# Kernel tuning notes

Measured on AMD Instinct MI355X. Metric: run time of the kernel, lower is better.

Reference implementation:

```python
import jax, jax.numpy as jnp
import numpy as np

D_MODEL = 768
N_HEADS = 12
D_HEAD = D_MODEL // N_HEADS
D_FF = 3072
EPS = 1e-5


def setup_inputs() -> dict:
    key = jax.random.key(0)
    ks = jax.random.split(key, 12)
    s = 0.02
    return {
        "x": jax.random.normal(ks[0], (2, 2048, D_MODEL), dtype=jnp.float32),
        "ln1_g": jnp.ones((D_MODEL,), jnp.float32),
        "ln1_b": jnp.zeros((D_MODEL,), jnp.float32),
        "ln2_g": jnp.ones((D_MODEL,), jnp.float32),
        "ln2_b": jnp.zeros((D_MODEL,), jnp.float32),
        "w_qkv": jax.random.normal(ks[1], (D_MODEL, 3 * D_MODEL), jnp.float32) * s,
        "b_qkv": jnp.zeros((3 * D_MODEL,), jnp.float32),
        "w_out": jax.random.normal(ks[2], (D_MODEL, D_MODEL), jnp.float32) * s,
        "b_out": jnp.zeros((D_MODEL,), jnp.float32),
        "w_fc1": jax.random.normal(ks[3], (D_MODEL, D_FF), jnp.float32) * s,
        "b_fc1": jnp.zeros((D_FF,), jnp.float32),
        "w_fc2": jax.random.normal(ks[4], (D_FF, D_MODEL), jnp.float32) * s,
        "b_fc2": jnp.zeros((D_MODEL,), jnp.float32),
    }


def _layernorm(x, g, b):
    mu = jnp.mean(x, axis=-1, keepdims=True)
    var = jnp.var(x, axis=-1, keepdims=True)
    return (x - mu) * jax.lax.rsqrt(var + EPS) * g + b


def _attention(h, w_qkv, b_qkv, w_out, b_out):
    B, S, _ = h.shape
    qkv = h @ w_qkv + b_qkv  # [B,S,3D]
    qkv = qkv.reshape(B, S, 3, N_HEADS, D_HEAD)
    q, k, v = qkv[:, :, 0], qkv[:, :, 1], qkv[:, :, 2]  # [B,S,H,Dh]
    scale = 1.0 / np.sqrt(D_HEAD).astype(np.float32)
    scores = jnp.einsum("bqhd,bkhd->bhqk", q, k) * scale
    causal = jnp.tril(jnp.ones((S, S), bool))
    scores = jnp.where(causal[None, None], scores, -jnp.inf)
    attn = jax.nn.softmax(scores, axis=-1)
    out = jnp.einsum("bhqk,bkhd->bqhd", attn, v).reshape(B, S, D_MODEL)
    return out @ w_out + b_out


def reference(x, ln1_g, ln1_b, ln2_g, ln2_b, w_qkv, b_qkv, w_out, b_out,
              w_fc1, b_fc1, w_fc2, b_fc2):
    # x = x + Attention(LN1(x))
    x = x + _attention(_layernorm(x, ln1_g, ln1_b), w_qkv, b_qkv, w_out, b_out)
    # x = x + FFN(LN2(x)); GELU is exact (erf) to match torch nn.GELU default
    h = _layernorm(x, ln2_g, ln2_b)
    h = jax.nn.gelu(h @ w_fc1 + b_fc1, approximate=False) @ w_fc2 + b_fc2
    return x + h
```

## Files before the change

### kernel.cpp

```cpp
#include <hip/hip_runtime.h>
#include <hip/hip_bf16.h>

typedef unsigned short u16;
typedef unsigned int u32;
typedef unsigned char u8;
using short8 = __attribute__((ext_vector_type(8))) short;
using f32x4  = __attribute__((ext_vector_type(4))) float;
using float4v = __attribute__((ext_vector_type(4))) float;

__device__ __forceinline__ u16 f2bf(float f) {
    __hip_bfloat16 h = __float2bfloat16(f);
    union { __hip_bfloat16 h; u16 u; } cv; cv.h = h; return cv.u;
}
__device__ __forceinline__ float bf2f(u16 u) {
    union { u32 u; float f; } cv; cv.u = ((u32)u) << 16; return cv.f;
}
__device__ __forceinline__ u16 f2bf_trunc(float f) {
    union { float f; u32 u; } cv; cv.f = f; return (u16)(cv.u >> 16);
}

__device__ __forceinline__ void gload_lds16(const void* g, void* l) {
    __builtin_amdgcn_global_load_lds(
        (const __attribute__((address_space(1))) u32*)g,
        (__attribute__((address_space(3))) u32*)l, 16, 0, 0);
}

__device__ __forceinline__ int xcd_remap(int flat, int nwg) {
    int q = nwg >> 3, r = nwg & 7;
    int xcd = flat & 7, pos = flat >> 3;
    int start = xcd < r ? xcd * (q + 1) : r * (q + 1) + (xcd - r) * q;
    return start + pos;
}

__global__ __launch_bounds__(256) void transpose_w(const float* __restrict__ W,
                                                   u16* __restrict__ Wt, int K, int N) {
    __shared__ float tile[32][33];
    int n0 = blockIdx.x * 32, k0 = blockIdx.y * 32;
    int tx = threadIdx.x & 31, ty = threadIdx.x >> 5;
    for (int i = 0; i < 4; i++) {
        int k = ty + i * 8;
        tile[k][tx] = W[(long)(k0 + k) * N + n0 + tx];
    }
    __syncthreads();
    for (int i = 0; i < 4; i++) {
        int n = ty + i * 8;
        Wt[(long)(n0 + n) * K + k0 + tx] = f2bf(tile[tx][n]);
    }
}

__global__ __launch_bounds__(256) void transpose_v(const u16* __restrict__ qkv,
                                                   u16* __restrict__ Vt) {
    __shared__ u16 tile[64][72];
    int s0 = blockIdx.x * 64;
    int bh = blockIdx.y;
    int b = bh / 12, h = bh % 12;
    int tid = threadIdx.x;
    const u16* src = qkv + (long)b * 2048 * 2304 + 1536 + h * 64;
    #pragma unroll
    for (int j = 0; j < 2; ++j) {
        int c = tid + j * 256;
        int srow = c >> 3, ch = c & 7;
        *(short8*)&tile[srow][ch * 8] = *(const short8*)(src + (long)(s0 + srow) * 2304 + ch * 8);
    }
    __syncthreads();
    u16* dst = Vt + (long)bh * 64 * 2048 + s0;
    #pragma unroll
    for (int j = 0; j < 2; ++j) {
        int c = tid + j * 256;
        int d = c >> 3, ch = c & 7;
        short8 v;
        #pragma unroll
        for (int e = 0; e < 8; ++e) v[e] = (short)tile[ch * 8 + e][d];
        *(short8*)(dst + (long)d * 2048 + ch * 8) = v;
    }
}

__global__ __launch_bounds__(256) void ln_kernel(const float* __restrict__ x,
                                                 const float* __restrict__ gain,
                                                 const float* __restrict__ beta,
                                                 u16* __restrict__ out) {
    int row = blockIdx.x;
    const float* xr = x + (long)row * 768;
    int tid = threadIdx.x;
    float v[3];
    float s = 0.f, s2 = 0.f;
    for (int j = 0; j < 3; j++) {
        v[j] = xr[tid + 256 * j];
        s += v[j]; s2 += v[j] * v[j];
    }
    for (int off = 32; off; off >>= 1) {
        s  += __shfl_down(s, off);
        s2 += __shfl_down(s2, off);
    }
    __shared__ float ws[8];
    int lane = tid & 63, w = tid >> 6;
    if (lane == 0) { ws[w] = s; ws[4 + w] = s2; }
    __syncthreads();
    s  = ws[0] + ws[1] + ws[2] + ws[3];
    s2 = ws[4] + ws[5] + ws[6] + ws[7];
    float mu  = s * (1.f / 768.f);
    float var = s2 * (1.f / 768.f) - mu * mu;
    float rs  = rsqrtf(var + 1e-5f);
    for (int j = 0; j < 3; j++) {
        int c = tid + 256 * j;
        out[(long)row * 768 + c] = f2bf((v[j] - mu) * rs * gain[c] + beta[c]);
    }
}

template <int EPI>
__global__ __launch_bounds__(256) void gemm_bf16(const u16* __restrict__ A, int lda,
                                                 const u16* __restrict__ Bt, int ldb,
                                                 const float* __restrict__ bias,
                                                 const float* __restrict__ res,
                                                 void* __restrict__ Cout0,
                                                 void* __restrict__ Cout1,
                                                 int M, int N, int K, int nN) {
    __shared__ alignas(16) u16 As[2][128 * 32];
    __shared__ alignas(16) u16 Bs[2][128 * 32];
    int nwg = gridDim.x;
    int wgid = xcd_remap(blockIdx.x, nwg);
    int tN = (wgid % nN) * 128, tM = (wgid / nN) * 128;
    int z = blockIdx.z;
    const u16* Ab = A + (long)z * K;
    const u16* Bb = Bt + (long)z * K;
    void* Cw = z ? Cout1 : Cout0;
    int tid = threadIdx.x;
    int wid = tid >> 6, lane = tid & 63;
    int wm = wid >> 1, wn = wid & 1;
    int g = lane >> 4, r = lane & 15;
    int srow = tid >> 2;
    int scol = tid & 3;

    f32x4 acc[4][4] = {};
    int KT = K >> 5;

    auto stage = [&](int kt) {
        int k0 = kt << 5;
        u16* ab = As[kt & 1];
        u16* bb = Bs[kt & 1];
        #pragma unroll
        for (int j = 0; j < 2; ++j) {
            int row = j * 64 + srow;
            int slot = scol ^ (row & 3);
            gload_lds16(Ab + (long)(tM + row) * lda + k0 + slot * 8, ab + (j * 64 + wid * 16) * 32);
            gload_lds16(Bb + (long)(tN + row) * ldb + k0 + slot * 8, bb + (j * 64 + wid * 16) * 32);
        }
    };

    stage(0);
    for (int kt = 0; kt < KT; ++kt) {
        if (kt + 1 < KT) {
            stage(kt + 1);
            asm volatile("s_waitcnt vmcnt(4)" ::: "memory");
        } else {
            asm volatile("s_waitcnt vmcnt(0)" ::: "memory");
        }
        __builtin_amdgcn_sched_barrier(0);
        __builtin_amdgcn_s_barrier();
        const u16* ab = As[kt & 1];
        const u16* bb = Bs[kt & 1];

        short8 af[4], bf[4];
        #pragma unroll
        for (int mi = 0; mi < 4; ++mi) {
            int row = wm * 64 + mi * 16 + r;
            af[mi] = *(const short8*)(ab + row * 32 + ((g ^ (row & 3)) * 8));
        }
        #pragma unroll
        for (int ni = 0; ni < 4; ++ni) {
            int row = wn * 64 + ni * 16 + r;
            bf[ni] = *(const short8*)(bb + row * 32 + ((g ^ (row & 3)) * 8));
        }
        #pragma unroll
        for (int mi = 0; mi < 4; ++mi)
            #pragma unroll
            for (int ni = 0; ni < 4; ++ni)
                acc[mi][ni] = __builtin_amdgcn_mfma_f32_16x16x32_bf16(af[mi], bf[ni], acc[mi][ni], 0, 0, 0);
        __builtin_amdgcn_s_barrier();
    }

    #pragma unroll
    for (int mi = 0; mi < 4; mi++) {
        #pragma unroll
        for (int ni = 0; ni < 4; ni++) {
            int col = tN + wn * 64 + ni * 16 + r;
            float bv = (EPI == 3) ? 0.f : bias[col];
            #pragma unroll
            for (int reg = 0; reg < 4; reg++) {
                int row = tM + wm * 64 + mi * 16 + g * 4 + reg;
                float v = acc[mi][ni][reg] + bv;
                if (EPI == 1) {
                    v += res[(long)row * N + col];
                    ((float*)Cw)[(long)row * N + col] = v;
                } else if (EPI == 2) {
                    v = 0.5f * v * (1.f + erff(v * 0.70710678118f));
                    ((u16*)Cw)[(long)row * N + col] = f2bf(v);
                } else if (EPI == 3) {
                    ((float*)Cw)[(long)row * N + col] = v;
                } else {
                    ((u16*)Cw)[(long)row * N + col] = f2bf(v);
                }
            }
        }
    }
}

__global__ __launch_bounds__(192) void fc2_combine(const float* __restrict__ P0,
                                                   const float* __restrict__ P1,
                                                   const float* __restrict__ bias,
                                                   const float* __restrict__ res,
                                                   float* __restrict__ out) {
    long row = blockIdx.x;
    int c = threadIdx.x * 4;
    long i = row * 768 + c;
    float4v a = *(const float4v*)(P0 + i);
    float4v b = *(const float4v*)(P1 + i);
    float4v bs = *(const float4v*)(bias + c);
    float4v rr = *(const float4v*)(res + i);
    float4v o = a + b + bs + rr;
    *(float4v*)(out + i) = o;
}

__device__ __constant__ u8 SLOT_QI[40] = {
    15,15,15,15, 14,14,14, 13,13,13, 12,12,12, 11,11,11, 10,10, 9,9, 8,8, 7,7, 6, 5, 4, 3,
    14,10,6,2,  13,9,5,1,  12,8,4,0 };
__device__ __constant__ u8 SLOT_C[40] = {
    0,1,2,3, 0,1,2, 0,1,2, 0,1,2, 0,1,2, 0,1, 0,1, 0,1, 0,1, 0, 0, 0, 0,
    3,2,1,0, 3,2,1,0, 3,2,1,0 };

__global__ __launch_bounds__(256) void attn_kernel(const u16* __restrict__ qkv,
                                                   const u16* __restrict__ Vt,
                                                   u16* __restrict__ Opart,
                                                   float* __restrict__ Ml) {
    __shared__ alignas(16) u16 Ks[2 * 64 * 64];
    __shared__ alignas(16) u16 Vs[2 * 64 * 64];
    __shared__ alignas(16) u16 Ps[4 * 32 * 64];
    int flat = blockIdx.x;
    int s = flat / 24, bh = flat % 24;
    int qi = SLOT_QI[s], c = SLOT_C[s];
    int b = bh / 12, h = bh % 12;
    int tid = threadIdx.x;
    int w = tid >> 6, lane = tid & 63;
    int g = lane >> 4, r = lane & 15;
    int qt0 = qi * 128;
    int qw0 = qt0 + w * 32;
    int kvbase = c * 512;
    int nit = (c < (qi >> 2)) ? 8 : (2 * (qi & 3) + 2);
    const u16* base = qkv + (long)b * 2048 * 2304;
    const u16* Qb = base + h * 64;
    const u16* Kb = base + 768 + h * 64;
    const u16* Vtb = Vt + (long)bh * 64 * 2048;

    const float SC = 0.125f * 1.44269504f;
    short8 qf[2][2];
    #pragma unroll
    for (int fi = 0; fi < 2; ++fi) {
        const u16* qrow = Qb + (long)(qw0 + fi * 16 + r) * 2304;
        qf[fi][0] = *(const short8*)(qrow + 8 * g);
        qf[fi][1] = *(const short8*)(qrow + 32 + 8 * g);
        #pragma unroll
        for (int kh = 0; kh < 2; ++kh)
            #pragma unroll
            for (int j = 0; j < 8; ++j)
                qf[fi][kh][j] = (short)f2bf(bf2f((u16)qf[fi][kh][j]) * SC);
    }

    f32x4 oacc[2][4] = {};
    float mrow[2][4], psum[2][4];
    #pragma unroll
    for (int fi = 0; fi < 2; ++fi)
        #pragma unroll
        for (int i = 0; i < 4; i++) { mrow[fi][i] = 8.0f; psum[fi][i] = 0.f; }

    auto stage = [&](int kt) {
        int kv0 = kvbase + kt * 64;
        u16* kb = Ks + (kt & 1) * 4096;
        u16* vb = Vs + (kt & 1) * 4096;
        #pragma unroll
        for (int j = 0; j < 2; ++j) {
            int cc = w * 128 + j * 64 + lane;
            int row = cc >> 3;
            int slot = (cc & 7) ^ (row & 7);
            gload_lds16(Kb + (long)(kv0 + row) * 2304 + slot * 8, kb + (w * 128 + j * 64) * 8);
            gload_lds16(Vtb + (long)row * 2048 + kv0 + slot * 8, vb + (w * 128 + j * 64) * 8);
        }
    };

    stage(0);
    for (int kt = 0; kt < nit; ++kt) {
        int kv0 = kvbase + kt * 64;
        if (kt + 1 < nit) {
            stage(kt + 1);
            asm volatile("s_waitcnt vmcnt(4)" ::: "memory");
        } else {
            asm volatile("s_waitcnt vmcnt(0)" ::: "memory");
        }
        __builtin_amdgcn_sched_barrier(0);
        __builtin_amdgcn_s_barrier();
        const u16* kb = Ks + (kt & 1) * 4096;
        const u16* vb = Vs + (kt & 1) * 4096;

        bool act0 = kv0 <= qw0 + 15;
        bool act1 = kv0 <= qw0 + 31;

        f32x4 sc[2][4] = {};
        if (act1) {
            #pragma unroll
            for (int nt = 0; nt < 4; ++nt)
                #pragma unroll
                for (int kh = 0; kh < 2; ++kh) {
                    short8 bk = *(const short8*)(kb + (nt * 16 + r) * 64 + ((kh * 32 + g * 8) ^ ((r & 7) << 3)));
                    sc[1][nt] = __builtin_amdgcn_mfma_f32_16x16x32_bf16(qf[1][kh], bk, sc[1][nt], 0, 0, 0);
                    if (act0)
                        sc[0][nt] = __builtin_amdgcn_mfma_f32_16x16x32_bf16(qf[0][kh], bk, sc[0][nt], 0, 0, 0);
                }

            #pragma unroll
            for (int fi = 0; fi < 2; ++fi) {
                if (fi == 0 && !act0) continue;
                if ((kv0 + 63) > (qw0 + fi * 16)) {
                    #pragma unroll
                    for (int nt = 0; nt < 4; ++nt)
                        #pragma unroll
                        for (int reg = 0; reg < 4; ++reg)
                            if ((kv0 + nt * 16 + r) > (qw0 + fi * 16 + g * 4 + reg))
                                sc[fi][nt][reg] = -1e30f;
                }
            }

            float tl[2][4];
            bool need = false;
            #pragma unroll
            for (int fi = 0; fi < 2; ++fi) {
                if (fi == 0 && !act0) continue;
                #pragma unroll
                for (int reg = 0; reg < 4; ++reg) {
                    tl[fi][reg] = fmaxf(fmaxf(sc[fi][0][reg], sc[fi][1][reg]),
                                        fmaxf(sc[fi][2][reg], sc[fi][3][reg]));
                    need = need || (tl[fi][reg] > mrow[fi][reg] + 8.f);
                }
            }
            if (__any(need)) {
                #pragma unroll
                for (int fi = 0; fi < 2; ++fi) {
                    if (fi == 0 && !act0) continue;
                    #pragma unroll
                    for (int reg = 0; reg < 4; ++reg) {
                        float rm = tl[fi][reg];
                        #pragma unroll
                        for (int off = 1; off < 16; off <<= 1)
                            rm = fmaxf(rm, __shfl_xor(rm, off));
                        float mnew = fmaxf(mrow[fi][reg], rm);
                        float alpha = exp2f(mrow[fi][reg] - mnew);
                        mrow[fi][reg] = mnew;
                        psum[fi][reg] *= alpha;
                        #pragma unroll
                        for (int dt = 0; dt < 4; ++dt) oacc[fi][dt][reg] *= alpha;
                    }
                }
            }

            #pragma unroll
            for (int fi = 0; fi < 2; ++fi) {
                if (fi == 0 && !act0) continue;
                u16* Pw = Ps + (w * 32 + fi * 16) * 64;
                #pragma unroll
                for (int nt = 0; nt < 4; ++nt)
                    #pragma unroll
                    for (int reg = 0; reg < 4; ++reg) {
                        float p = exp2f(sc[fi][nt][reg] - mrow[fi][reg]);
                        psum[fi][reg] += p;
                        int row = g * 4 + reg;
                        Pw[row * 64 + ((nt * 16 + r) ^ ((row & 7) << 3))] = f2bf_trunc(p);
                    }
            }

            short8 pf[2][2];
            #pragma unroll
            for (int fi = 0; fi < 2; ++fi) {
                if (fi == 0 && !act0) continue;
                const u16* Pw = Ps + (w * 32 + fi * 16) * 64;
                pf[fi][0] = *(const short8*)(Pw + r * 64 + ((g * 8) ^ ((r & 7) << 3)));
                pf[fi][1] = *(const short8*)(Pw + r * 64 + ((32 + g * 8) ^ ((r & 7) << 3)));
            }
            #pragma unroll
            for (int dt = 0; dt < 4; ++dt)
                #pragma unroll
                for (int kc = 0; kc < 2; ++kc) {
                    short8 vf = *(const short8*)(vb + (dt * 16 + r) * 64 + ((kc * 32 + g * 8) ^ ((r & 7) << 3)));
                    oacc[1][dt] = __builtin_amdgcn_mfma_f32_16x16x32_bf16(pf[1][kc], vf, oacc[1][dt], 0, 0, 0);
                    if (act0)
                        oacc[0][dt] = __builtin_amdgcn_mfma_f32_16x16x32_bf16(pf[0][kc], vf, oacc[0][dt], 0, 0, 0);
                }
        }
        __builtin_amdgcn_s_barrier();
    }

    float lrow[2][4];
    #pragma unroll
    for (int fi = 0; fi < 2; ++fi)
        #pragma unroll
        for (int reg = 0; reg < 4; ++reg) {
            float l = psum[fi][reg];
            #pragma unroll
            for (int off = 1; off < 16; off <<= 1)
                l += __shfl_xor(l, off);
            lrow[fi][reg] = l;
        }

    long pbase = ((long)c * 24 + bh) * 2048;
    #pragma unroll
    for (int fi = 0; fi < 2; ++fi)
        #pragma unroll
        for (int dt = 0; dt < 4; ++dt)
            #pragma unroll
            for (int reg = 0; reg < 4; ++reg) {
                int q = qw0 + fi * 16 + g * 4 + reg;
                int d = dt * 16 + r;
                Opart[(pbase + q) * 64 + d] = f2bf(oacc[fi][dt][reg]);
            }
    if (r == 0) {
        #pragma unroll
        for (int fi = 0; fi < 2; ++fi)
            #pragma unroll
            for (int reg = 0; reg < 4; ++reg) {
                int q = qw0 + fi * 16 + g * 4 + reg;
                Ml[(pbase + q) * 2]     = mrow[fi][reg];
                Ml[(pbase + q) * 2 + 1] = lrow[fi][reg];
            }
    }
}

__global__ __launch_bounds__(256) void attn_combine(const u16* __restrict__ Opart,
                                                    const float* __restrict__ Ml,
                                                    u16* __restrict__ Ob) {
    int bh = blockIdx.y;
    int b = bh / 12, h = bh % 12;
    int q = blockIdx.x * 4 + (threadIdx.x >> 6);
    int d = threadIdx.x & 63;
    int qi = q >> 7;
    int nact = (qi >> 2) + 1;
    float mv[4], lv[4];
    float M = -1e30f;
    for (int c = 0; c < nact; ++c) {
        long base = ((long)c * 24 + bh) * 2048 + q;
        mv[c] = Ml[base * 2];
        lv[c] = Ml[base * 2 + 1];
        M = fmaxf(M, mv[c]);
    }
    float denom = 0.f, val = 0.f;
    for (int c = 0; c < nact; ++c) {
        float wgt = exp2f(mv[c] - M);
        denom += lv[c] * wgt;
        val += wgt * bf2f(Opart[(((long)c * 24 + bh) * 2048 + q) * 64 + d]);
    }
    Ob[((long)b * 2048 + q) * 768 + h * 64 + d] = f2bf(val / denom);
}

extern "C" void kernel_launch(void* const* d_in, const int* in_sizes, int n_in,
                              void* d_out, int out_size, void* d_ws, size_t ws_size,
                              hipStream_t stream) {
    const float* x     = (const float*)d_in[0];
    const float* ln1_g = (const float*)d_in[1];
    const float* ln1_b = (const float*)d_in[2];
    const float* ln2_g = (const float*)d_in[3];
    const float* ln2_b = (const float*)d_in[4];
    const float* w_qkv = (const float*)d_in[5];
    const float* b_qkv = (const float*)d_in[6];
    const float* w_out = (const float*)d_in[7];
    const float* b_out = (const float*)d_in[8];
    const float* w_fc1 = (const float*)d_in[9];
    const float* b_fc1 = (const float*)d_in[10];
    const float* w_fc2 = (const float*)d_in[11];
    const float* b_fc2 = (const float*)d_in[12];

    char* ws = (char*)d_ws;
    size_t off = 0;
    auto alloc = [&](size_t bytes) { void* p = ws + off; off += (bytes + 255) & ~255ULL; return p; };
    u16* h1    = (u16*)alloc(4096UL * 768 * 2);
    u16* WqkvT = (u16*)alloc(2304UL * 768 * 2);
    u16* WoutT = (u16*)alloc(768UL * 768 * 2);
    u16* Wfc1T = (u16*)alloc(3072UL * 768 * 2);
    u16* Wfc2T = (u16*)alloc(768UL * 3072 * 2);
    u16* qkvb  = (u16*)alloc(4096UL * 2304 * 2);
    u16* Vtb   = (u16*)alloc(24UL * 64 * 2048 * 2);
    u16* Ob    = (u16*)alloc(4096UL * 768 * 2);
    float* x2  = (float*)alloc(4096UL * 768 * 4);
    char* pool = (char*)alloc(4096UL * 768 * 2 + 4096UL * 3072 * 2);
    u16* h2      = (u16*)pool;
    u16* gbuf    = (u16*)(pool + 4096UL * 768 * 2);
    u16* Opart   = (u16*)pool;
    float* Ml    = (float*)(pool + 4UL * 24 * 2048 * 64 * 2);
    float* P0 = (float*)qkvb;
    float* P1 = (float*)h1;

    transpose_w<<<dim3(2304 / 32, 768 / 32), 256, 0, stream>>>(w_qkv, WqkvT, 768, 2304);
    transpose_w<<<dim3(768 / 32, 768 / 32), 256, 0, stream>>>(w_out, WoutT, 768, 768);
    transpose_w<<<dim3(3072 / 32, 768 / 32), 256, 0, stream>>>(w_fc1, Wfc1T, 768, 3072);
    transpose_w<<<dim3(768 / 32, 3072 / 32), 256, 0, stream>>>(w_fc2, Wfc2T, 3072, 768);

    ln_kernel<<<4096, 256, 0, stream>>>(x, ln1_g, ln1_b, h1);
    gemm_bf16<0><<<dim3(576, 1, 1), 256, 0, stream>>>(h1, 768, WqkvT, 768, b_qkv, nullptr, qkvb, nullptr, 4096, 2304, 768, 18);
    transpose_v<<<dim3(32, 24), 256, 0, stream>>>(qkvb, Vtb);
    attn_kernel<<<dim3(960), 256, 0, stream>>>(qkvb, Vtb, Opart, Ml);
    attn_combine<<<dim3(512, 24), 256, 0, stream>>>(Opart, Ml, Ob);
    gemm_bf16<1><<<dim3(192, 1, 1), 256, 0, stream>>>(Ob, 768, WoutT, 768, b_out, x, x2, nullptr, 4096, 768, 768, 6);
    ln_kernel<<<4096, 256, 0, stream>>>(x2, ln2_g, ln2_b, h2);
    gemm_bf16<2><<<dim3(768, 1, 1), 256, 0, stream>>>(h2, 768, Wfc1T, 768, b_fc1, nullptr, gbuf, nullptr, 4096, 3072, 768, 24);
    gemm_bf16<3><<<dim3(192, 1, 2), 256, 0, stream>>>(gbuf, 3072, Wfc2T, 3072, nullptr, nullptr, P0, P1, 4096, 768, 1536, 6);
    fc2_combine<<<4096, 192, 0, stream>>>(P0, P1, b_fc2, x2, (float*)d_out);
}
```

Measured before the change: 216.0 us.

## Shrink GEMM M-tile to 64 rows and merge weight transposes into one launch

The bf16 GEMM tile changes from 128x128 to 64x128. Each wave now holds 2x4 accumulators instead of 4x4, and the A staging uses one 16-byte load per thread, so the wait count drops to vmcnt(3). Grid sizes double for all four GEMMs, which gives more workgroups and better fill across the CUs for these mid-sized matrices. The cost is lower arithmetic intensity per tile and more B-tile reloads. The four weight-transpose launches are also merged into one kernel that dispatches on block index, which removes launch overhead.

Result: slower. 223.1 us (+3.3%).

```diff
diff --git a/kernel.cpp b/kernel.cpp
--- a/kernel.cpp
+++ b/kernel.cpp
@@ -32,10 +32,23 @@
     return start + pos;
 }
 
-__global__ __launch_bounds__(256) void transpose_w(const float* __restrict__ W,
-                                                   u16* __restrict__ Wt, int K, int N) {
+__global__ __launch_bounds__(256) void transpose_all(const float* __restrict__ Wq,
+                                                     const float* __restrict__ Wo,
+                                                     const float* __restrict__ Wf1,
+                                                     const float* __restrict__ Wf2,
+                                                     u16* __restrict__ Tq,
+                                                     u16* __restrict__ To,
+                                                     u16* __restrict__ Tf1,
+                                                     u16* __restrict__ Tf2) {
     __shared__ float tile[32][33];
-    int n0 = blockIdx.x * 32, k0 = blockIdx.y * 32;
+    int id = blockIdx.x;
+    const float* W; u16* Wt; int K, N, local;
+    if (id < 1728)      { W = Wq;  Wt = Tq;  K = 768;  N = 2304; local = id; }
+    else if (id < 2304) { W = Wo;  Wt = To;  K = 768;  N = 768;  local = id - 1728; }
+    else if (id < 4608) { W = Wf1; Wt = Tf1; K = 768;  N = 3072; local = id - 2304; }
+    else                { W = Wf2; Wt = Tf2; K = 3072; N = 768;  local = id - 4608; }
+    int bx = N >> 5;
+    int n0 = (local % bx) * 32, k0 = (local / bx) * 32;
     int tx = threadIdx.x & 31, ty = threadIdx.x >> 5;
     for (int i = 0; i < 4; i++) {
         int k = ty + i * 8;
@@ -115,11 +128,11 @@
                                                  void* __restrict__ Cout0,
                                                  void* __restrict__ Cout1,
                                                  int M, int N, int K, int nN) {
-    __shared__ alignas(16) u16 As[2][128 * 32];
+    __shared__ alignas(16) u16 As[2][64 * 32];
     __shared__ alignas(16) u16 Bs[2][128 * 32];
     int nwg = gridDim.x;
     int wgid = xcd_remap(blockIdx.x, nwg);
-    int tN = (wgid % nN) * 128, tM = (wgid / nN) * 128;
+    int tN = (wgid % nN) * 128, tM = (wgid / nN) * 64;
     int z = blockIdx.z;
     const u16* Ab = A + (long)z * K;
     const u16* Bb = Bt + (long)z * K;
@@ -128,22 +141,25 @@
     int wid = tid >> 6, lane = tid & 63;
     int wm = wid >> 1, wn = wid & 1;
     int g = lane >> 4, r = lane & 15;
-    int srow = tid >> 2;
-    int scol = tid & 3;
-
-    f32x4 acc[4][4] = {};
+
+    f32x4 acc[2][4] = {};
     int KT = K >> 5;
 
     auto stage = [&](int kt) {
         int k0 = kt << 5;
         u16* ab = As[kt & 1];
         u16* bb = Bs[kt & 1];
+        {
+            int rowA = tid >> 2;
+            int slotA = (tid & 3) ^ (rowA & 3);
+            gload_lds16(Ab + (long)(tM + rowA) * lda + k0 + slotA * 8, ab + tid * 8);
+        }
         #pragma unroll
         for (int j = 0; j < 2; ++j) {
-            int row = j * 64 + srow;
-            int slot = scol ^ (row & 3);
-            gload_lds16(Ab + (long)(tM + row) * lda + k0 + slot * 8, ab + (j * 64 + wid * 16) * 32);
-            gload_lds16(Bb + (long)(tN + row) * ldb + k0 + slot * 8, bb + (j * 64 + wid * 16) * 32);
+            int c = j * 256 + tid;
+            int rowB = c >> 2;
+            int slotB = (c & 3) ^ (rowB & 3);
+            gload_lds16(Bb + (long)(tN + rowB) * ldb + k0 + slotB * 8, bb + c * 8);
         }
     };
 
@@ -151,7 +167,7 @@
     for (int kt = 0; kt < KT; ++kt) {
         if (kt + 1 < KT) {
             stage(kt + 1);
-            asm volatile("s_waitcnt vmcnt(4)" ::: "memory");
+            asm volatile("s_waitcnt vmcnt(3)" ::: "memory");
         } else {
             asm volatile("s_waitcnt vmcnt(0)" ::: "memory");
         }
@@ -160,10 +176,10 @@
         const u16* ab = As[kt & 1];
         const u16* bb = Bs[kt & 1];
 
-        short8 af[4], bf[4];
-        #pragma unroll
-        for (int mi = 0; mi < 4; ++mi) {
-            int row = wm * 64 + mi * 16 + r;
+        short8 af[2], bf[4];
+        #pragma unroll
+        for (int mi = 0; mi < 2; ++mi) {
+            int row = wm * 32 + mi * 16 + r;
             af[mi] = *(const short8*)(ab + row * 32 + ((g ^ (row & 3)) * 8));
         }
         #pragma unroll
@@ -172,7 +188,7 @@
             bf[ni] = *(const short8*)(bb + row * 32 + ((g ^ (row & 3)) * 8));
         }
         #pragma unroll
-        for (int mi = 0; mi < 4; ++mi)
+        for (int mi = 0; mi < 2; ++mi)
             #pragma unroll
             for (int ni = 0; ni < 4; ++ni)
                 acc[mi][ni] = __builtin_amdgcn_mfma_f32_16x16x32_bf16(af[mi], bf[ni], acc[mi][ni], 0, 0, 0);
@@ -180,14 +196,14 @@
     }
 
     #pragma unroll
-    for (int mi = 0; mi < 4; mi++) {
+    for (int mi = 0; mi < 2; mi++) {
         #pragma unroll
         for (int ni = 0; ni < 4; ni++) {
             int col = tN + wn * 64 + ni * 16 + r;
             float bv = (EPI == 3) ? 0.f : bias[col];
             #pragma unroll
             for (int reg = 0; reg < 4; reg++) {
-                int row = tM + wm * 64 + mi * 16 + g * 4 + reg;
+                int row = tM + wm * 32 + mi * 16 + g * 4 + reg;
                 float v = acc[mi][ni][reg] + bv;
                 if (EPI == 1) {
                     v += res[(long)row * N + col];
@@ -494,19 +510,17 @@
     float* P0 = (float*)qkvb;
     float* P1 = (float*)h1;
 
-    transpose_w<<<dim3(2304 / 32, 768 / 32), 256, 0, stream>>>(w_qkv, WqkvT, 768, 2304);
-    transpose_w<<<dim3(768 / 32, 768 / 32), 256, 0, stream>>>(w_out, WoutT, 768, 768);
-    transpose_w<<<dim3(3072 / 32, 768 / 32), 256, 0, stream>>>(w_fc1, Wfc1T, 768, 3072);
-    transpose_w<<<dim3(768 / 32, 3072 / 32), 256, 0, stream>>>(w_fc2, Wfc2T, 3072, 768);
+    transpose_all<<<dim3(6912), 256, 0, stream>>>(w_qkv, w_out, w_fc1, w_fc2,
+                                                  WqkvT, WoutT, Wfc1T, Wfc2T);
 
     ln_kernel<<<4096, 256, 0, stream>>>(x, ln1_g, ln1_b, h1);
-    gemm_bf16<0><<<dim3(576, 1, 1), 256, 0, stream>>>(h1, 768, WqkvT, 768, b_qkv, nullptr, qkvb, nullptr, 4096, 2304, 768, 18);
+    gemm_bf16<0><<<dim3(1152, 1, 1), 256, 0, stream>>>(h1, 768, WqkvT, 768, b_qkv, nullptr, qkvb, nullptr, 4096, 2304, 768, 18);
     transpose_v<<<dim3(32, 24), 256, 0, stream>>>(qkvb, Vtb);
     attn_kernel<<<dim3(960), 256, 0, stream>>>(qkvb, Vtb, Opart, Ml);
     attn_combine<<<dim3(512, 24), 256, 0, stream>>>(Opart, Ml, Ob);
-    gemm_bf16<1><<<dim3(192, 1, 1), 256, 0, stream>>>(Ob, 768, WoutT, 768, b_out, x, x2, nullptr, 4096, 768, 768, 6);
+    gemm_bf16<1><<<dim3(384, 1, 1), 256, 0, stream>>>(Ob, 768, WoutT, 768, b_out, x, x2, nullptr, 4096, 768, 768, 6);
     ln_kernel<<<4096, 256, 0, stream>>>(x2, ln2_g, ln2_b, h2);
-    gemm_bf16<2><<<dim3(768, 1, 1), 256, 0, stream>>>(h2, 768, Wfc1T, 768, b_fc1, nullptr, gbuf, nullptr, 4096, 3072, 768, 24);
-    gemm_bf16<3><<<dim3(192, 1, 2), 256, 0, stream>>>(gbuf, 3072, Wfc2T, 3072, nullptr, nullptr, P0, P1, 4096, 768, 1536, 6);
+    gemm_bf16<2><<<dim3(1536, 1, 1), 256, 0, stream>>>(h2, 768, Wfc1T, 768, b_fc1, nullptr, gbuf, nullptr, 4096, 3072, 768, 24);
+    gemm_bf16<3><<<dim3(384, 1, 2), 256, 0, stream>>>(gbuf, 3072, Wfc2T, 3072, nullptr, nullptr, P0, P1, 4096, 768, 1536, 6);
     fc2_combine<<<4096, 192, 0, stream>>>(P0, P1, b_fc2, x2, (float*)d_out);
 }
```

## Triple-buffer GEMM LDS staging and merge weight transposes into one launch

Applied to the files above, without the earlier changes.

The bf16 GEMM now keeps three LDS stages instead of two, prefetching two k-tiles ahead with a matching vmcnt wait. This is meant to hide more global-load latency behind MFMA work. Separately, the four weight-transpose launches are merged into one kernel that routes blocks by flat index, cutting launch overhead. The extra LDS stage raises per-block shared memory to 48KB, which may lower occupancy.

Result: faster. 209.2 us (-3.1%).

```diff
diff --git a/kernel.cpp b/kernel.cpp
--- a/kernel.cpp
+++ b/kernel.cpp
@@ -32,10 +32,23 @@
     return start + pos;
 }
 
-__global__ __launch_bounds__(256) void transpose_w(const float* __restrict__ W,
-                                                   u16* __restrict__ Wt, int K, int N) {
+__global__ __launch_bounds__(256) void transpose_all(const float* __restrict__ Wq,
+                                                     const float* __restrict__ Wo,
+                                                     const float* __restrict__ Wf1,
+                                                     const float* __restrict__ Wf2,
+                                                     u16* __restrict__ Tq,
+                                                     u16* __restrict__ To,
+                                                     u16* __restrict__ Tf1,
+                                                     u16* __restrict__ Tf2) {
     __shared__ float tile[32][33];
-    int n0 = blockIdx.x * 32, k0 = blockIdx.y * 32;
+    int id = blockIdx.x;
+    const float* W; u16* Wt; int K, N, local;
+    if (id < 1728)      { W = Wq;  Wt = Tq;  K = 768;  N = 2304; local = id; }
+    else if (id < 2304) { W = Wo;  Wt = To;  K = 768;  N = 768;  local = id - 1728; }
+    else if (id < 4608) { W = Wf1; Wt = Tf1; K = 768;  N = 3072; local = id - 2304; }
+    else                { W = Wf2; Wt = Tf2; K = 3072; N = 768;  local = id - 4608; }
+    int bx = N >> 5;
+    int n0 = (local % bx) * 32, k0 = (local / bx) * 32;
     int tx = threadIdx.x & 31, ty = threadIdx.x >> 5;
     for (int i = 0; i < 4; i++) {
         int k = ty + i * 8;
@@ -115,8 +128,8 @@
                                                  void* __restrict__ Cout0,
                                                  void* __restrict__ Cout1,
                                                  int M, int N, int K, int nN) {
-    __shared__ alignas(16) u16 As[2][128 * 32];
-    __shared__ alignas(16) u16 Bs[2][128 * 32];
+    __shared__ alignas(16) u16 As[3][128 * 32];
+    __shared__ alignas(16) u16 Bs[3][128 * 32];
     int nwg = gridDim.x;
     int wgid = xcd_remap(blockIdx.x, nwg);
     int tN = (wgid % nN) * 128, tM = (wgid / nN) * 128;
@@ -134,10 +147,10 @@
     f32x4 acc[4][4] = {};
     int KT = K >> 5;
 
-    auto stage = [&](int kt) {
+    auto stage = [&](int kt, int buf) {
         int k0 = kt << 5;
-        u16* ab = As[kt & 1];
-        u16* bb = Bs[kt & 1];
+        u16* ab = As[buf];
+        u16* bb = Bs[buf];
         #pragma unroll
         for (int j = 0; j < 2; ++j) {
             int row = j * 64 + srow;
@@ -147,18 +160,24 @@
         }
     };
 
-    stage(0);
+    stage(0, 0);
+    stage(1, 1);
+    int sb = 2, cb = 0;
     for (int kt = 0; kt < KT; ++kt) {
-        if (kt + 1 < KT) {
-            stage(kt + 1);
+        if (kt + 2 < KT) {
+            stage(kt + 2, sb);
+            if (++sb == 3) sb = 0;
+            asm volatile("s_waitcnt vmcnt(8)" ::: "memory");
+        } else if (kt + 1 < KT) {
             asm volatile("s_waitcnt vmcnt(4)" ::: "memory");
         } else {
             asm volatile("s_waitcnt vmcnt(0)" ::: "memory");
         }
         __builtin_amdgcn_sched_barrier(0);
         __builtin_amdgcn_s_barrier();
-        const u16* ab = As[kt & 1];
-        const u16* bb = Bs[kt & 1];
+        const u16* ab = As[cb];
+        const u16* bb = Bs[cb];
+        if (++cb == 3) cb = 0;
 
         short8 af[4], bf[4];
         #pragma unroll
@@ -494,10 +513,8 @@
     float* P0 = (float*)qkvb;
     float* P1 = (float*)h1;
 
-    transpose_w<<<dim3(2304 / 32, 768 / 32), 256, 0, stream>>>(w_qkv, WqkvT, 768, 2304);
-    transpose_w<<<dim3(768 / 32, 768 / 32), 256, 0, stream>>>(w_out, WoutT, 768, 768);
-    transpose_w<<<dim3(3072 / 32, 768 / 32), 256, 0, stream>>>(w_fc1, Wfc1T, 768, 3072);
-    transpose_w<<<dim3(768 / 32, 3072 / 32), 256, 0, stream>>>(w_fc2, Wfc2T, 3072, 768);
+    transpose_all<<<dim3(6912), 256, 0, stream>>>(w_qkv, w_out, w_fc1, w_fc2,
+                                                  WqkvT, WoutT, Wfc1T, Wfc2T);
 
     ln_kernel<<<4096, 256, 0, stream>>>(x, ln1_g, ln1_b, h1);
     gemm_bf16<0><<<dim3(576, 1, 1), 256, 0, stream>>>(h1, 768, WqkvT, 768, b_qkv, nullptr, qkvb, nullptr, 4096, 2304, 768, 18);
```
